# Kernel optimization log

Measured on AMD Instinct MI355X. Metric: run time of the kernel, lower is better.

Reference implementation:

```python
import jax, jax.numpy as jnp
import numpy as np

N_NODES = 100000
N_EDGES = 1600000
IN_F = 16
OUT_F = 64
PERIODS = 12
N_PHASE = 4


def setup_inputs() -> dict:
    key = jax.random.key(0)
    ks = jax.random.split(key, 12)
    inp = {
        'x': jax.random.normal(ks[0], (N_NODES, IN_F, PERIODS), jnp.float32),
        'edge_index': jax.random.randint(ks[1], (2, N_EDGES), 0, N_NODES, jnp.int64),
        'attn': jax.random.normal(ks[2], (PERIODS,), jnp.float32),
        'conv_z_w': jax.random.normal(ks[3], (IN_F, OUT_F), jnp.float32) * 0.1,
        'conv_z_b': jnp.zeros((OUT_F,), jnp.float32),
        'conv_r_w': jax.random.normal(ks[4], (IN_F, OUT_F), jnp.float32) * 0.1,
        'conv_r_b': jnp.zeros((OUT_F,), jnp.float32),
        'conv_h_w': jax.random.normal(ks[5], (IN_F, OUT_F), jnp.float32) * 0.1,
        'conv_h_b': jnp.zeros((OUT_F,), jnp.float32),
        'lin_z_w': jax.random.normal(ks[6], (2 * OUT_F, OUT_F), jnp.float32) * 0.1,
        'lin_z_b': jnp.zeros((OUT_F,), jnp.float32),
        'lin_r_w': jax.random.normal(ks[7], (2 * OUT_F, OUT_F), jnp.float32) * 0.1,
        'lin_r_b': jnp.zeros((OUT_F,), jnp.float32),
        'lin_h_w': jax.random.normal(ks[8], (2 * OUT_F, OUT_F), jnp.float32) * 0.1,
        'lin_h_b': jnp.zeros((OUT_F,), jnp.float32),
        'out_w': jax.random.normal(ks[9], (OUT_F, N_PHASE), jnp.float32) * 0.1,
        'out_b': jnp.zeros((N_PHASE,), jnp.float32),
    }
    return inp


def _gcn_norm(edge_index, num_nodes, dtype):
    # add self loops (fill value 1), symmetric normalization as in PyG gcn_norm
    loops = jnp.arange(num_nodes, dtype=edge_index.dtype)
    src = jnp.concatenate([edge_index[0], loops])
    dst = jnp.concatenate([edge_index[1], loops])
    deg = jax.ops.segment_sum(jnp.ones_like(dst, dtype=dtype), dst, num_segments=num_nodes)
    dinv = jnp.where(deg > 0, jax.lax.rsqrt(deg), jnp.zeros_like(deg))
    norm = dinv[src] * dinv[dst]  # [E + N]
    return src, dst, norm


def reference(x, edge_index, attn, conv_z_w, conv_z_b, conv_r_w, conv_r_b,
              conv_h_w, conv_h_b, lin_z_w, lin_z_b, lin_r_w, lin_r_b,
              lin_h_w, lin_h_b, out_w, out_b):
    N = x.shape[0]
    periods = x.shape[2]
    F_out = conv_z_w.shape[1]
    src, dst, norm = _gcn_norm(edge_index, N, x.dtype)

    def conv(Xp, W, b):
        XW = Xp @ W                                   # [N, F_out]
        msg = norm[:, None] * XW[src]                 # gather over edges
        return jax.ops.segment_sum(msg, dst, num_segments=N) + b

    probs = jax.nn.softmax(attn)
    H0 = jnp.zeros((N, F_out), x.dtype)  # A3TGCN never carries H between periods
    H_accum = jnp.zeros((N, F_out), x.dtype)
    for p in range(periods):
        Xp = x[:, :, p]
        Z = jax.nn.sigmoid(jnp.concatenate([conv(Xp, conv_z_w, conv_z_b), H0], axis=1) @ lin_z_w + lin_z_b)
        R = jax.nn.sigmoid(jnp.concatenate([conv(Xp, conv_r_w, conv_r_b), H0], axis=1) @ lin_r_w + lin_r_b)
        Ht = jnp.tanh(jnp.concatenate([conv(Xp, conv_h_w, conv_h_b), H0 * R], axis=1) @ lin_h_w + lin_h_b)
        H = Z * H0 + (1.0 - Z) * Ht
        H_accum = H_accum + probs[p] * H

    h = jax.nn.relu(H_accum)
    logits = h @ out_w + out_b
    return jax.nn.softmax(logits, axis=1)
```

## Files before the change

kernel.cpp:

```cpp
#include <hip/hip_runtime.h>
#include <math.h>

#define NN 100000
#define NE 1600000
#define PERIODS 12
#define SLOTS 48
#define NBUCK 391
#define FRAG 256
#define CAPB 48
#define PTH 512

typedef unsigned short ushort_t;
typedef __attribute__((ext_vector_type(8))) short short8;
typedef __attribute__((ext_vector_type(16))) float floatx16;
typedef __attribute__((ext_vector_type(2))) float f32x2;

union F4S8 { float4 f; short8 s; int4 i; };

__device__ __forceinline__ ushort_t f2bf(float f) {
  unsigned u = __float_as_uint(f);
  unsigned r = u + 0x7fffu + ((u >> 16) & 1u);
  return (ushort_t)(r >> 16);
}

__device__ __forceinline__ f32x2 unpk(unsigned u) {
  f32x2 t;
  t.x = __uint_as_float(u << 16);
  t.y = __uint_as_float(u & 0xffff0000u);
  return t;
}
__device__ __forceinline__ void pkadd(f32x2& a, f32x2 t) {
  asm("v_pk_add_f32 %0, %0, %1" : "+v"(a) : "v"(t));
}

__global__ __launch_bounds__(PTH) void k_part(
    const int* __restrict__ src, const int* __restrict__ dst,
    int* __restrict__ cnt_blk, int* __restrict__ part,
    const float* __restrict__ attn,
    const float* __restrict__ czw, const float* __restrict__ czb,
    const float* __restrict__ chw, const float* __restrict__ chb,
    const float* __restrict__ lzw, const float* __restrict__ lzb,
    const float* __restrict__ lhw, const float* __restrict__ lhb,
    ushort_t* __restrict__ Bz32, ushort_t* __restrict__ Bh32,
    float2* __restrict__ cb2, float* __restrict__ probs_ext) {
  if (blockIdx.x == FRAG) {
    for (int t5 = threadIdx.x; t5 < 1024; t5 += PTH) {
      int f = t5 >> 6, c = t5 & 63;
      float az = 0.f, ah = 0.f;
#pragma unroll 8
      for (int k = 0; k < 64; ++k) {
        az += czw[f * 64 + k] * lzw[k * 64 + c];
        ah += chw[f * 64 + k] * lhw[k * 64 + c];
      }
      int idx = (((c >> 5) * 64) + ((f >> 3) * 32) + (c & 31)) * 8 + (f & 7);
      Bz32[idx] = f2bf(az);
      Bh32[idx] = f2bf(ah);
    }
    if (threadIdx.x < 64) {
      int t = threadIdx.x;
      float vz = lzb[t], vh = lhb[t];
      for (int k = 0; k < 64; ++k) {
        vz += czb[k] * lzw[k * 64 + t];
        vh += chb[k] * lhw[k * 64 + t];
      }
      cb2[t] = make_float2(vz, vh);
    }
    if (threadIdx.x == 0) {
      float m = -1e30f;
      for (int p = 0; p < PERIODS; ++p) m = fmaxf(m, attn[p]);
      float e[PERIODS], s = 0.f;
      for (int p = 0; p < PERIODS; ++p) { e[p] = __expf(attn[p] - m); s += e[p]; }
      float inv = 1.f / s;
      for (int r = 0; r < 32; ++r)
        probs_ext[r] = (r < 12) ? e[r] * inv : ((r < 24) ? e[r - 12] * inv : 0.f);
    }
    return;
  }
  __shared__ int cnt[NBUCK];
  int tid = threadIdx.x, blk = blockIdx.x;
  for (int c = tid; c < NBUCK; c += PTH) cnt[c] = 0;
  __syncthreads();
  for (unsigned i = blk * (unsigned)PTH + tid; i < NE / 4; i += FRAG * (unsigned)PTH) {
    int4 dv = ((const int4*)dst)[i];
    int4 sv = ((const int4*)src)[i];
    int d[4] = {dv.x, dv.y, dv.z, dv.w};
    int s[4] = {sv.x, sv.y, sv.z, sv.w};
#pragma unroll
    for (int k = 0; k < 4; ++k) {
      int cls = d[k] >> 8;
      int slot = atomicAdd(&cnt[cls], 1);
      if (slot < CAPB)
        part[(size_t)(cls * FRAG + blk) * CAPB + slot] = (d[k] & 255) | (s[k] << 8);
    }
  }
  __syncthreads();
  for (int c = tid; c < NBUCK; c += PTH) cnt_blk[blk * NBUCK + c] = cnt[c];
}

__global__ __launch_bounds__(512) void k_csr(const int* __restrict__ cnt_blk,
                                             const int* __restrict__ part,
                                             int* __restrict__ deg,
                                             int* __restrict__ csr) {
  __shared__ int cnt[256];
  int b = blockIdx.x, tid = threadIdx.x;
  if (tid < 256) cnt[tid] = 0;
  __syncthreads();
  int f = tid & 255, sub = tid >> 8;
  int c = cnt_blk[f * NBUCK + b];
  c = c < CAPB ? c : CAPB;
  const int* cell = part + (size_t)(b * FRAG + f) * CAPB;
  for (int i = sub; i < c; i += 2) {
    int r = cell[i];
    int dl = r & 255;
    int slot = atomicAdd(&cnt[dl], 1);
    if (slot < SLOTS)
      csr[((size_t)(b * 256 + dl)) * SLOTS + slot] = (r >> 8) * 384;
  }
  __syncthreads();
  int node = b * 256 + tid;
  if (tid < 256 && node < NN) {
    int cc = cnt[tid];
    deg[node] = cc;
    int cl = cc < SLOTS ? cc : SLOTS;
    int padded = (cl + 3) & ~3;
    int* row = csr + (size_t)node * SLOTS;
    for (int sl = cl; sl < padded; ++sl) row[sl] = NN * 384;
  }
}

__global__ __launch_bounds__(256) void k_prescale(const float* __restrict__ x,
                                                  const int* __restrict__ deg,
                                                  ushort_t* __restrict__ xs) {
  __shared__ float st[4][192];
  int wid = threadIdx.x >> 6, l = threadIdx.x & 63;
  int n = blockIdx.x * 4 + wid;
  if (n > NN || l >= 48) return;
  char* ob = (char*)xs;
  if (n == NN) {
    uint2 z; z.x = 0u; z.y = 0u;
    *(uint2*)(ob + (size_t)NN * 384 + l * 8) = z;
    return;
  }
  float4 v4 = *(const float4*)(x + (size_t)n * 192 + 4 * l);
  *(float4*)&st[wid][4 * l] = v4;
  asm volatile("s_waitcnt lgkmcnt(0)" ::: "memory");
  float dn = rsqrtf((float)(deg[n] + 1));
  float v[4];
#pragma unroll
  for (int c = 0; c < 4; ++c) {
    int o = 4 * l + c;
    v[c] = dn * st[wid][(o & 15) * 12 + (o >> 4)];
  }
  uint2 w;
  w.x = (unsigned)f2bf(v[0]) | ((unsigned)f2bf(v[1]) << 16);
  w.y = (unsigned)f2bf(v[2]) | ((unsigned)f2bf(v[3]) << 16);
  *(uint2*)(ob + (size_t)n * 384 + l * 8) = w;
}

__global__ __launch_bounds__(256) void k_main(
    const ushort_t* __restrict__ xs, const int* __restrict__ csr,
    const int* __restrict__ deg,
    const ushort_t* __restrict__ Bz32, const ushort_t* __restrict__ Bh32,
    const float2* __restrict__ cb2, const float* __restrict__ probs_ext,
    const float* __restrict__ out_w, const float* __restrict__ out_b,
    float* __restrict__ out) {
  __shared__ ushort_t Alds[4][32][16];
  int wid = __builtin_amdgcn_readfirstlane(threadIdx.x >> 6);
  int l = threadIdx.x & 63;
  int nA = blockIdx.x * 8 + wid * 2;
  int nB = nA + 1;
  char* albase = (char*)&Alds[wid][0][0];
  if (l < 16) *(int4*)(albase + 768 + l * 16) = make_int4(0, 0, 0, 0);

  const char* xb = (const char*)xs;
  unsigned loff = (unsigned)(l < 48 ? l : 47) * 8u;

  int2 dd = *(const int2*)(deg + nA);
  int dA = dd.x, dB = dd.y;
  int cA = dA < SLOTS ? dA : SLOTS, cB = dB < SLOTS ? dB : SLOTS;
  int KA = (cA + 3) >> 2, KB = (cB + 3) >> 2;
  const int* bktA = csr + (size_t)nA * SLOTS;
  const int* bktB = bktA + SLOTS;

  uint2 sA = *(const uint2*)(xb + (unsigned)nA * 384u + loff);
  uint2 sB = *(const uint2*)(xb + (unsigned)nB * 384u + loff);
  f32x2 aA01 = unpk(sA.x), aA23 = unpk(sA.y);
  f32x2 aB01 = unpk(sB.x), aB23 = unpk(sB.y);

  uint2 qa[4], qb[4];
  auto issue4 = [&](const int* bkt, int k, uint2* q) {
    int4 e = ((const int4*)bkt)[k];
    q[0] = *(const uint2*)(xb + (unsigned)e.x + loff);
    q[1] = *(const uint2*)(xb + (unsigned)e.y + loff);
    q[2] = *(const uint2*)(xb + (unsigned)e.z + loff);
    q[3] = *(const uint2*)(xb + (unsigned)e.w + loff);
  };
  auto accA4 = [&](const uint2* q) {
#pragma unroll
    for (int j = 0; j < 4; ++j) { pkadd(aA01, unpk(q[j].x)); pkadd(aA23, unpk(q[j].y)); }
  };
  auto accB4 = [&](const uint2* q) {
#pragma unroll
    for (int j = 0; j < 4; ++j) { pkadd(aB01, unpk(q[j].x)); pkadd(aB23, unpk(q[j].y)); }
  };

  int km = KA < KB ? KA : KB;
  int k = 0;
  for (; k < km; ++k) {
    issue4(bktA, k, qa);
    issue4(bktB, k, qb);
    accA4(qa);
    accB4(qb);
  }
  for (; k < KA; ++k) { issue4(bktA, k, qa); accA4(qa); }
  for (; k < KB; ++k) { issue4(bktB, k, qb); accB4(qb); }

  float dnA = rsqrtf((float)(dA + 1)), dnB = rsqrtf((float)(dB + 1));

  if (l < 48) {
    uint2 wA, wB;
    wA.x = (unsigned)f2bf(dnA * aA01.x) | ((unsigned)f2bf(dnA * aA01.y) << 16);
    wA.y = (unsigned)f2bf(dnA * aA23.x) | ((unsigned)f2bf(dnA * aA23.y) << 16);
    wB.x = (unsigned)f2bf(dnB * aB01.x) | ((unsigned)f2bf(dnB * aB01.y) << 16);
    wB.y = (unsigned)f2bf(dnB * aB23.x) | ((unsigned)f2bf(dnB * aB23.y) << 16);
    *(uint2*)(albase + l * 8) = wA;
    *(uint2*)(albase + 384 + l * 8) = wB;
  }
  asm volatile("s_waitcnt lgkmcnt(0)" ::: "memory");
  F4S8 afr;
  afr.f = *(const float4*)(albase + (unsigned)(l & 31) * 32u + (unsigned)(l >> 5) * 16u);

  F4S8 bz0, bz1, bh0, bh1;
  bz0.f = ((const float4*)Bz32)[l];
  bz1.f = ((const float4*)Bz32)[64 + l];
  bh0.f = ((const float4*)Bh32)[l];
  bh1.f = ((const float4*)Bh32)[64 + l];

  floatx16 zero16;
#pragma unroll
  for (int r = 0; r < 16; ++r) zero16[r] = 0.f;
  floatx16 az0 = __builtin_amdgcn_mfma_f32_32x32x16_bf16(afr.s, bz0.s, zero16, 0, 0, 0);
  floatx16 az1 = __builtin_amdgcn_mfma_f32_32x32x16_bf16(afr.s, bz1.s, zero16, 0, 0, 0);
  floatx16 ah0 = __builtin_amdgcn_mfma_f32_32x32x16_bf16(afr.s, bh0.s, zero16, 0, 0, 0);
  floatx16 ah1 = __builtin_amdgcn_mfma_f32_32x32x16_bf16(afr.s, bh1.s, zero16, 0, 0, 0);

  float2 cbv0 = cb2[l & 31], cbv1 = cb2[(l & 31) + 32];
  float prv[12];
  unsigned sby = (l & 32u) >> 1;
#pragma unroll
  for (int r = 0; r < 12; ++r) {
    const int rb = (r & 3) + 8 * (r >> 2);
    prv[r] = *(const float*)((const char*)probs_ext + rb * 4 + sby);
  }
  bool sh = (l & 32) != 0;
  float hA[2], hB[2];
#pragma unroll
  for (int t = 0; t < 2; ++t) {
    float g0 = 0.f, g1 = 0.f, g2 = 0.f;
    float2 cbv = t ? cbv1 : cbv0;
#pragma unroll
    for (int r = 0; r < 12; ++r) {
      float zz = (t ? az1[r] : az0[r]) + cbv.x;
      float hh = (t ? ah1[r] : ah0[r]) + cbv.y;
      float ez = __expf(zz);
      float e2h = __expf(2.f * hh);
      float val = (e2h - 1.f) * __builtin_amdgcn_rcpf((1.f + ez) * (e2h + 1.f));
      float c = prv[r] * val;
      if ((r >> 2) == 0) g0 += c;
      else if ((r >> 2) == 1) g1 += c;
      else g2 += c;
    }
    float pa = g0 + (sh ? 0.f : g1);
    float pb = g2 + (sh ? g1 : 0.f);
    pa += __shfl_xor(pa, 32, 64);
    pb += __shfl_xor(pb, 32, 64);
    hA[t] = fmaxf(pa, 0.f);
    hB[t] = fmaxf(pb, 0.f);
  }

  int c0 = l & 31;
  float4 w0 = ((const float4*)out_w)[c0];
  float4 w1 = ((const float4*)out_w)[c0 + 32];
  float h0 = sh ? hB[0] : hA[0];
  float h1 = sh ? hB[1] : hA[1];
  float l0 = h0 * w0.x; l0 = fmaf(h1, w1.x, l0);
  float l1 = h0 * w0.y; l1 = fmaf(h1, w1.y, l1);
  float l2 = h0 * w0.z; l2 = fmaf(h1, w1.z, l2);
  float l3 = h0 * w0.w; l3 = fmaf(h1, w1.w, l3);
#pragma unroll
  for (int o = 1; o < 32; o <<= 1) {
    l0 += __shfl_xor(l0, o, 64);
    l1 += __shfl_xor(l1, o, 64);
    l2 += __shfl_xor(l2, o, 64);
    l3 += __shfl_xor(l3, o, 64);
  }
  l0 += out_b[0]; l1 += out_b[1]; l2 += out_b[2]; l3 += out_b[3];
  float m = fmaxf(fmaxf(l0, l1), fmaxf(l2, l3));
  float e0 = __expf(l0 - m), e1 = __expf(l1 - m), e2 = __expf(l2 - m), e3 = __expf(l3 - m);
  float inv = __builtin_amdgcn_rcpf(e0 + e1 + e2 + e3);
  if (c0 < 4) {
    float v = (c0 == 0) ? e0 * inv : (c0 == 1) ? e1 * inv : (c0 == 2) ? e2 * inv : e3 * inv;
    out[(size_t)(sh ? nB : nA) * 4 + c0] = v;
  }
}

extern "C" void kernel_launch(void* const* d_in, const int* in_sizes, int n_in,
                              void* d_out, int out_size, void* d_ws, size_t ws_size,
                              hipStream_t stream) {
  const float* x    = (const float*)d_in[0];
  const int*   ei   = (const int*)d_in[1];
  const float* attn = (const float*)d_in[2];
  const float* czw  = (const float*)d_in[3];
  const float* czb  = (const float*)d_in[4];
  const float* chw  = (const float*)d_in[7];
  const float* chb  = (const float*)d_in[8];
  const float* lzw  = (const float*)d_in[9];
  const float* lzb  = (const float*)d_in[10];
  const float* lhw  = (const float*)d_in[13];
  const float* lhb  = (const float*)d_in[14];
  const float* outw = (const float*)d_in[15];
  const float* outb = (const float*)d_in[16];
  float* out = (float*)d_out;

  char* ws = (char*)d_ws;
  size_t off = 0;
  auto alloc = [&](size_t bytes) {
    void* p = ws + off;
    off += (bytes + 255) & ~(size_t)255;
    return p;
  };
  int*      deg       = (int*)alloc((size_t)NN * 4);
  int*      csr       = (int*)alloc((size_t)NN * SLOTS * 4);
  void*     shared_region = alloc((size_t)(NN + 1) * 192 * 2);
  int*      part      = (int*)shared_region;
  ushort_t* xs        = (ushort_t*)shared_region;
  int*      cnt_blk   = (int*)alloc((size_t)FRAG * NBUCK * 4);
  ushort_t* Bz32      = (ushort_t*)alloc(2 * 64 * 8 * 2);
  ushort_t* Bh32      = (ushort_t*)alloc(2 * 64 * 8 * 2);
  float2*   cb2       = (float2*)alloc(64 * 8);
  float*    probs_ext = (float*)alloc(32 * 4);

  k_part<<<FRAG + 1, PTH, 0, stream>>>(ei, ei + NE, cnt_blk, part,
                                       attn, czw, czb, chw, chb,
                                       lzw, lzb, lhw, lhb,
                                       Bz32, Bh32, cb2, probs_ext);
  k_csr<<<NBUCK, 512, 0, stream>>>(cnt_blk, part, deg, csr);
  k_prescale<<<NN / 4 + 1, 256, 0, stream>>>(x, deg, xs);
  k_main<<<NN / 8, 256, 0, stream>>>(xs, csr, deg, Bz32, Bh32, cb2, probs_ext,
                                     outw, outb, out);
}
```

Measured before the change: 298.9 us.

## Fuse feature prescale into CSR build and align partition buffer per bucket

The separate prescale kernel is folded into the CSR kernel. Each bucket block now prescales its own 256 nodes right after building their CSR rows, using the degree counts already held in shared memory instead of reading deg back from global memory. The partition buffer is re-laid out with a fixed per-bucket stride, so each block's bf16 output region covers exactly the partition region it has just consumed, which keeps the shared aliasing safe. The partition kernel's thread count is also halved. The cost is less parallelism for the prescale work: only 391 blocks remain, and each wave processes 32 nodes one after another.

Result: slower. 312.8 us (+4.6%).

```diff
diff --git a/kernel.cpp b/kernel.cpp
--- a/kernel.cpp
+++ b/kernel.cpp
@@ -8,7 +8,8 @@
 #define NBUCK 391
 #define FRAG 256
 #define CAPB 48
-#define PTH 512
+#define PTH 256
+#define PSTR 24576
 
 typedef unsigned short ushort_t;
 typedef __attribute__((ext_vector_type(8))) short short8;
@@ -90,25 +91,47 @@
       int cls = d[k] >> 8;
       int slot = atomicAdd(&cnt[cls], 1);
       if (slot < CAPB)
-        part[(size_t)(cls * FRAG + blk) * CAPB + slot] = (d[k] & 255) | (s[k] << 8);
+        part[(size_t)cls * PSTR + blk * CAPB + slot] = (d[k] & 255) | (s[k] << 8);
     }
   }
   __syncthreads();
   for (int c = tid; c < NBUCK; c += PTH) cnt_blk[blk * NBUCK + c] = cnt[c];
 }
 
-__global__ __launch_bounds__(512) void k_csr(const int* __restrict__ cnt_blk,
-                                             const int* __restrict__ part,
-                                             int* __restrict__ deg,
-                                             int* __restrict__ csr) {
+__device__ __forceinline__ void prescale_node(const float* __restrict__ x,
+                                              ushort_t* __restrict__ xs,
+                                              float* stw, int n, int cc, int l) {
+  float4 v4 = *(const float4*)(x + (size_t)n * 192 + 4 * l);
+  *(float4*)&stw[4 * l] = v4;
+  asm volatile("s_waitcnt lgkmcnt(0)" ::: "memory");
+  float dn = rsqrtf((float)(cc + 1));
+  float v[4];
+#pragma unroll
+  for (int c = 0; c < 4; ++c) {
+    int o = 4 * l + c;
+    v[c] = dn * stw[(o & 15) * 12 + (o >> 4)];
+  }
+  uint2 w;
+  w.x = (unsigned)f2bf(v[0]) | ((unsigned)f2bf(v[1]) << 16);
+  w.y = (unsigned)f2bf(v[2]) | ((unsigned)f2bf(v[3]) << 16);
+  *(uint2*)((char*)xs + (size_t)n * 384 + l * 8) = w;
+}
+
+__global__ __launch_bounds__(512) void k_csr_ps(const int* __restrict__ cnt_blk,
+                                                const int* __restrict__ part,
+                                                int* __restrict__ deg,
+                                                int* __restrict__ csr,
+                                                const float* __restrict__ x,
+                                                ushort_t* __restrict__ xs) {
   __shared__ int cnt[256];
+  __shared__ float st[8][192];
   int b = blockIdx.x, tid = threadIdx.x;
   if (tid < 256) cnt[tid] = 0;
   __syncthreads();
   int f = tid & 255, sub = tid >> 8;
   int c = cnt_blk[f * NBUCK + b];
   c = c < CAPB ? c : CAPB;
-  const int* cell = part + (size_t)(b * FRAG + f) * CAPB;
+  const int* cell = part + (size_t)b * PSTR + f * CAPB;
   for (int i = sub; i < c; i += 2) {
     int r = cell[i];
     int dl = r & 255;
@@ -126,35 +149,19 @@
     int* row = csr + (size_t)node * SLOTS;
     for (int sl = cl; sl < padded; ++sl) row[sl] = NN * 384;
   }
-}
-
-__global__ __launch_bounds__(256) void k_prescale(const float* __restrict__ x,
-                                                  const int* __restrict__ deg,
-                                                  ushort_t* __restrict__ xs) {
-  __shared__ float st[4][192];
-  int wid = threadIdx.x >> 6, l = threadIdx.x & 63;
-  int n = blockIdx.x * 4 + wid;
-  if (n > NN || l >= 48) return;
-  char* ob = (char*)xs;
-  if (n == NN) {
+  int wv = tid >> 6, l = tid & 63;
+  if (b == 0 && tid < 48) {
     uint2 z; z.x = 0u; z.y = 0u;
-    *(uint2*)(ob + (size_t)NN * 384 + l * 8) = z;
-    return;
-  }
-  float4 v4 = *(const float4*)(x + (size_t)n * 192 + 4 * l);
-  *(float4*)&st[wid][4 * l] = v4;
-  asm volatile("s_waitcnt lgkmcnt(0)" ::: "memory");
-  float dn = rsqrtf((float)(deg[n] + 1));
-  float v[4];
-#pragma unroll
-  for (int c = 0; c < 4; ++c) {
-    int o = 4 * l + c;
-    v[c] = dn * st[wid][(o & 15) * 12 + (o >> 4)];
-  }
-  uint2 w;
-  w.x = (unsigned)f2bf(v[0]) | ((unsigned)f2bf(v[1]) << 16);
-  w.y = (unsigned)f2bf(v[2]) | ((unsigned)f2bf(v[3]) << 16);
-  *(uint2*)(ob + (size_t)n * 384 + l * 8) = w;
+    *(uint2*)((char*)xs + (size_t)NN * 384 + tid * 8) = z;
+  }
+  if (l >= 48) return;
+  float* stw = st[wv];
+  for (int j = 0; j < 32; ++j) {
+    int idx = wv * 32 + j;
+    int n = b * 256 + idx;
+    if (n >= NN) break;
+    prescale_node(x, xs, stw, n, cnt[idx], l);
+  }
 }
 
 __global__ __launch_bounds__(256) void k_main(
@@ -329,11 +336,11 @@
     off += (bytes + 255) & ~(size_t)255;
     return p;
   };
-  int*      deg       = (int*)alloc((size_t)NN * 4);
-  int*      csr       = (int*)alloc((size_t)NN * SLOTS * 4);
-  void*     shared_region = alloc((size_t)(NN + 1) * 192 * 2);
-  int*      part      = (int*)shared_region;
-  ushort_t* xs        = (ushort_t*)shared_region;
+  int* deg = (int*)alloc((size_t)NN * 4);
+  int* csr = (int*)alloc((size_t)NN * SLOTS * 4);
+  void* shared_region = alloc((size_t)NBUCK * PSTR * 4);
+  int*      part = (int*)shared_region;
+  ushort_t* xs   = (ushort_t*)shared_region;
   int*      cnt_blk   = (int*)alloc((size_t)FRAG * NBUCK * 4);
   ushort_t* Bz32      = (ushort_t*)alloc(2 * 64 * 8 * 2);
   ushort_t* Bh32      = (ushort_t*)alloc(2 * 64 * 8 * 2);
@@ -344,8 +351,7 @@
                                        attn, czw, czb, chw, chb,
                                        lzw, lzb, lhw, lhb,
                                        Bz32, Bh32, cb2, probs_ext);
-  k_csr<<<NBUCK, 512, 0, stream>>>(cnt_blk, part, deg, csr);
-  k_prescale<<<NN / 4 + 1, 256, 0, stream>>>(x, deg, xs);
+  k_csr_ps<<<NBUCK, 512, 0, stream>>>(cnt_blk, part, deg, csr, x, xs);
   k_main<<<NN / 8, 256, 0, stream>>>(xs, csr, deg, Bz32, Bh32, cb2, probs_ext,
                                      outw, outb, out);
 }
```
